# Optimization experiments

Measured on AMD Instinct MI355X. Metric: run time of the kernel, lower is better.

Reference implementation:

```python
import jax, jax.numpy as jnp
import numpy as np

B, C, H, W = 8, 384, 32, 32
KEYS, HEADS, U = 16, 4, 1
VS = C // HEADS
N = H * W
BN_EPS = 1e-5


def setup_inputs() -> dict:
    key = jax.random.key(0)
    ks = jax.random.split(key, 8)
    x = jax.random.normal(ks[0], (B, C, H, W), dtype=jnp.float32)
    # 1x1 convs (spectral-normalized in torch; SN only rescales the weight,
    # so a plain weight matrix computes the same functional form)
    Wq = jax.random.normal(ks[1], (KEYS * HEADS, C), dtype=jnp.float32) * 0.02
    Wk = jax.random.normal(ks[2], (KEYS * U, C), dtype=jnp.float32) * 0.02
    Wv = jax.random.normal(ks[3], (VS * U, C), dtype=jnp.float32) * 0.02
    # BatchNorm affine params (torch code xavier-inits weight, zeros bias)
    gamma_q = jax.random.normal(ks[4], (KEYS * HEADS,), dtype=jnp.float32)
    beta_q = jnp.zeros((KEYS * HEADS,), dtype=jnp.float32)
    gamma_v = jax.random.normal(ks[5], (VS * U,), dtype=jnp.float32)
    beta_v = jnp.zeros((VS * U,), dtype=jnp.float32)
    pos_emb = jax.random.normal(ks[6], (N, N, KEYS, U), dtype=jnp.float32)
    return {"x": x, "Wq": Wq, "Wk": Wk, "Wv": Wv,
            "gamma_q": gamma_q, "beta_q": beta_q,
            "gamma_v": gamma_v, "beta_v": beta_v,
            "pos_emb": pos_emb}


def _bn(z, gamma, beta):
    # z: (B, Ch, N); BatchNorm2d in training mode: biased batch stats over (B, N)
    mean = jnp.mean(z, axis=(0, 2), keepdims=True)
    var = jnp.var(z, axis=(0, 2), keepdims=True)
    zn = (z - mean) * jax.lax.rsqrt(var + BN_EPS)
    return zn * gamma[None, :, None] + beta[None, :, None]


def reference(x, Wq, Wk, Wv, gamma_q, beta_q, gamma_v, beta_v, pos_emb):
    xf = x.reshape(B, C, N)                       # 1x1 conv == per-pixel matmul
    q = jnp.einsum('oc,bcn->bon', Wq, xf)         # (B, KEYS*HEADS, N)
    k = jnp.einsum('oc,bcn->bon', Wk, xf)         # (B, KEYS*U, N)
    v = jnp.einsum('oc,bcn->bon', Wv, xf)         # (B, VS*U, N)
    q = _bn(q, gamma_q, beta_q)
    v = _bn(v, gamma_v, beta_v)
    q = q.reshape(B, HEADS, KEYS, N)
    k = k.reshape(B, U, KEYS, N)
    v = v.reshape(B, U, VS, N)
    k = jax.nn.softmax(k, axis=-1)
    lambdac = jnp.einsum('bukm,buvm->bkv', k, v)          # content lambda
    Yc = jnp.einsum('bhkn,bkv->bhvn', q, lambdac)
    lambdap = jnp.einsum('nmku,buvm->bnkv', pos_emb, v)   # position lambda (B,N,K,V)
    Yp = jnp.einsum('bhkn,bnkv->bhvn', q, lambdap)
    Y = (Yc + Yp).reshape(B, C, H, W)
    return Y
```

## Files before the change

kernel.cpp:

```cpp
#include <hip/hip_runtime.h>

typedef __attribute__((ext_vector_type(8))) short short8;
typedef __attribute__((ext_vector_type(16))) float floatx16;
typedef __attribute__((ext_vector_type(4))) float floatx4;
typedef unsigned short ushort16_t;
typedef unsigned int uint32;

#define BB 8
#define CC 384
#define NPIX 1024
#define TOTCH 176
#define BN_EPS 1e-5f

__device__ __forceinline__ ushort16_t f2bf(float x) {
    uint32 u = __float_as_uint(x);
    u += 0x7FFFu + ((u >> 16) & 1u);
    return (ushort16_t)(u >> 16);
}
__device__ __forceinline__ uint32 pk2(float a, float b) {
    uint32 ua = __float_as_uint(a); ua += 0x7FFFu + ((ua >> 16) & 1u);
    uint32 ub = __float_as_uint(b); ub += 0x7FFFu + ((ub >> 16) & 1u);
    return (ua >> 16) | (ub & 0xFFFF0000u);
}
__device__ __forceinline__ int div48(int x) {
    return (int)(((unsigned)x * 21846u) >> 20);
}
#define LGKM0_ONLY 0xC07F


__global__ __launch_bounds__(256) void k_xt(const float* __restrict__ x,
    const float* __restrict__ Wq, const float* __restrict__ Wk,
    const float* __restrict__ Wv,
    ushort16_t* __restrict__ xbf, ushort16_t* __restrict__ wbf)
{
    int bx = blockIdx.x, t = threadIdx.x;
    if (bx < 256) {
        __shared__ __align__(16) ushort16_t T[32 * 392];
        int col0 = bx * 32;
        int b = col0 >> 10, nbase = col0 & 1023;
        const float* xb = x + (size_t)b * (CC * NPIX) + nbase;
        #pragma unroll
        for (int j = 0; j < 12; ++j) {
            int idx = t + 256 * j;
            int c = idx >> 3, ng = idx & 7;
            float4 f = *(const float4*)(xb + (size_t)c * NPIX + ng * 4);
            int n = ng * 4;
            T[(n + 0) * 392 + c] = f2bf(f.x);
            T[(n + 1) * 392 + c] = f2bf(f.y);
            T[(n + 2) * 392 + c] = f2bf(f.z);
            T[(n + 3) * 392 + c] = f2bf(f.w);
        }
        __syncthreads();
        #pragma unroll
        for (int j = 0; j < 6; ++j) {
            int task = t + 256 * j;
            int col = div48(task);
            int ch  = task - col * 48;
            uint4 w = *(const uint4*)&T[col * 392 + ch * 8];
            *(uint4*)&xbf[(size_t)(col0 + col) * CC + ch * 8] = w;
        }
    } else {
        #pragma unroll
        for (int jj = 0; jj < 9; ++jj) {
            int idx8 = ((bx - 256) * 9 + jj) * 256 + t;
            int row = div48(idx8);
            int g   = idx8 - row * 48;
            float4 f0, f1;
            if (row < 176) {
                const float* src;
                if (row < 64)       src = Wq + (size_t)row * CC;
                else if (row < 80)  src = Wk + (size_t)(row - 64) * CC;
                else                src = Wv + (size_t)(row - 80) * CC;
                f0 = *(const float4*)(src + g * 8);
                f1 = *(const float4*)(src + g * 8 + 4);
            } else {
                f0.x = f0.y = f0.z = f0.w = 0.f;
                f1 = f0;
            }
            uint4 w;
            w.x = pk2(f0.x, f0.y); w.y = pk2(f0.z, f0.w);
            w.z = pk2(f1.x, f1.y); w.w = pk2(f1.z, f1.w);
            *(uint4*)&wbf[(size_t)row * CC + g * 8] = w;
        }
    }
}

__global__ __launch_bounds__(256) void k_proj(const ushort16_t* __restrict__ xbf,
    const ushort16_t* __restrict__ wbf, float* __restrict__ qkv)
{
    int t = threadIdx.x;
    int wave = t >> 6, lane = t & 63;
    int ct = blockIdx.x * 4 + wave;
    int r0 = blockIdx.y * 16;
    int col = ct * 16 + (lane & 15);
    int kh  = lane >> 4;
    const ushort16_t* ap = wbf + (size_t)(r0 + (lane & 15)) * CC + kh * 8;
    const ushort16_t* bp = xbf + (size_t)col * CC + kh * 8;
    floatx4 acc = {0.f, 0.f, 0.f, 0.f};
    short8 a0 = *(const short8*)ap;
    short8 b0 = *(const short8*)bp;
    #pragma unroll
    for (int k = 1; k < 12; ++k) {
        short8 a1 = *(const short8*)(ap + k * 32);
        short8 b1 = *(const short8*)(bp + k * 32);
        acc = __builtin_amdgcn_mfma_f32_16x16x32_bf16(a0, b0, acc, 0, 0, 0);
        a0 = a1; b0 = b1;
    }
    acc = __builtin_amdgcn_mfma_f32_16x16x32_bf16(a0, b0, acc, 0, 0, 0);
    int b = col >> 10, n = col & 1023;
    #pragma unroll
    for (int r = 0; r < 4; ++r) {
        int ch = r0 + (lane >> 4) * 4 + r;
        qkv[((size_t)b * TOTCH + ch) * NPIX + n] = acc[r];
    }
}

__global__ __launch_bounds__(256) void k_bnsm(const float* __restrict__ qkv,
    const float* __restrict__ gq, const float* __restrict__ bq,
    const float* __restrict__ gv, const float* __restrict__ bv,
    float* __restrict__ sA, float* __restrict__ sB, float* __restrict__ ksm)
{
    int bx = blockIdx.x, tid = threadIdx.x;
    int wid = tid >> 6, lane = tid & 63;
    if (bx < 160) {
        int ch = bx;
        int row; float gamma, beta;
        if (ch < 64) { row = ch; gamma = gq[ch]; beta = bq[ch]; }
        else { int j = ch - 64; row = 80 + j; gamma = gv[j]; beta = bv[j]; }
        float s = 0.f, ss = 0.f;
        #pragma unroll
        for (int j = 0; j < 8; ++j) {
            int i4 = tid + 256 * j;
            int b = i4 >> 8, n4 = i4 & 255;
            float4 f = *(const float4*)(qkv + ((size_t)b * TOTCH + row) * NPIX
                                            + n4 * 4);
            s  += f.x + f.y + f.z + f.w;
            ss += f.x * f.x + f.y * f.y + f.z * f.z + f.w * f.w;
        }
        #pragma unroll
        for (int off = 32; off > 0; off >>= 1) {
            s  += __shfl_down(s, off);
            ss += __shfl_down(ss, off);
        }
        __shared__ float rs[4], rss[4];
        if (lane == 0) { rs[wid] = s; rss[wid] = ss; }
        __syncthreads();
        if (tid == 0) {
            float S  = rs[0] + rs[1] + rs[2] + rs[3];
            float SS = rss[0] + rss[1] + rss[2] + rss[3];
            float inv = 1.f / (BB * NPIX);
            float mean = S * inv;
            float var  = SS * inv - mean * mean;
            float a = gamma * rsqrtf(var + BN_EPS);
            sA[row] = a;
            sB[row] = beta - mean * a;
        }
    } else {
        int idx = bx - 160;
        int kc = idx & 15, b = idx >> 4;
        const float* rowp = qkv + ((size_t)b * TOTCH + 64 + kc) * NPIX;
        float4 v4 = *(const float4*)(rowp + tid * 4);
        float v[4] = {v4.x, v4.y, v4.z, v4.w};
        float mx = fmaxf(fmaxf(v[0], v[1]), fmaxf(v[2], v[3]));
        #pragma unroll
        for (int off = 32; off > 0; off >>= 1) mx = fmaxf(mx, __shfl_down(mx, off));
        __shared__ float sm[4], ssum[4];
        if (lane == 0) sm[wid] = mx;
        __syncthreads();
        mx = fmaxf(fmaxf(sm[0], sm[1]), fmaxf(sm[2], sm[3]));
        float e[4], s = 0.f;
        #pragma unroll
        for (int j = 0; j < 4; ++j) { e[j] = __expf(v[j] - mx); s += e[j]; }
        #pragma unroll
        for (int off = 32; off > 0; off >>= 1) s += __shfl_down(s, off);
        if (lane == 0) ssum[wid] = s;
        __syncthreads();
        float inv = 1.f / (ssum[0] + ssum[1] + ssum[2] + ssum[3]);
        float4 o;
        o.x = e[0] * inv; o.y = e[1] * inv; o.z = e[2] * inv; o.w = e[3] * inv;
        *(float4*)(ksm + ((size_t)b * 16 + kc) * NPIX + tid * 4) = o;
    }
}

__global__ __launch_bounds__(256) void k_packlc(const float* __restrict__ qkv,
    const float* __restrict__ sA, const float* __restrict__ sB,
    const float* __restrict__ ksm,
    ushort16_t* __restrict__ qt_g, ushort16_t* __restrict__ vt_g,
    ushort16_t* __restrict__ lc_g)
{
    int bx = blockIdx.x, t = threadIdx.x;
    if (bx < 128) {
        int bh = t & 31, nn = (t >> 5) & 7;
        int n = bx * 8 + nn;
        int b = bh >> 2, h = bh & 3;
        float vals[16];
        #pragma unroll
        for (int k = 0; k < 16; ++k) {
            int ch = h * 16 + k;
            vals[k] = qkv[((size_t)b * TOTCH + ch) * NPIX + n] * sA[ch] + sB[ch];
        }
        uint4 w0, w1;
        w0.x = pk2(vals[0], vals[1]);  w0.y = pk2(vals[2], vals[3]);
        w0.z = pk2(vals[4], vals[5]);  w0.w = pk2(vals[6], vals[7]);
        w1.x = pk2(vals[8], vals[9]);  w1.y = pk2(vals[10], vals[11]);
        w1.z = pk2(vals[12], vals[13]); w1.w = pk2(vals[14], vals[15]);
        *(uint4*)&qt_g[(size_t)n * 512 + bh * 8]       = w0;
        *(uint4*)&qt_g[(size_t)n * 512 + 256 + bh * 8] = w1;
    } else if (bx < 512) {
        int gi = (bx - 128) * 256 + t;
        int m8 = gi & 127;
        int vg = (gi >> 7) % 96;
        int b  = gi / (96 * 128);
        int m  = m8 * 8;
        int row = 80 + vg;
        float a = sA[row], bb = sB[row];
        const float* p = qkv + ((size_t)b * TOTCH + row) * NPIX + m;
        float4 f0 = *(const float4*)p;
        float4 f1 = *(const float4*)(p + 4);
        uint4 w;
        w.x = pk2(f0.x * a + bb, f0.y * a + bb);
        w.y = pk2(f0.z * a + bb, f0.w * a + bb);
        w.z = pk2(f1.x * a + bb, f1.y * a + bb);
        w.w = pk2(f1.z * a + bb, f1.w * a + bb);
        int mt = m >> 5, mq = (m >> 3) & 3;
        int vhh = vg / 48, vtt = (vg % 48) >> 4, vl = vg & 15;
        size_t idx = ((((size_t)b * 32 + mt) * 2 + vhh) * 3 + vtt) * 512
                   + mq * 128 + vl * 8;
        *(uint4*)&vt_g[idx] = w;
    } else {
        int gi = bx - 512;
        int v = gi % 96, b = gi / 96;
        int row = 80 + v;
        float a = sA[row], bb = sB[row];
        const float* vp = qkv + ((size_t)b * TOTCH + row) * NPIX;
        const float* kp = ksm + (size_t)b * 16 * NPIX;
        float4 vv = *(const float4*)(vp + t * 4);
        float4 vhat;
        vhat.x = vv.x * a + bb; vhat.y = vv.y * a + bb;
        vhat.z = vv.z * a + bb; vhat.w = vv.w * a + bb;
        float acc[16];
        #pragma unroll
        for (int k = 0; k < 16; ++k) {
            float4 kk = *(const float4*)(kp + (size_t)k * NPIX + t * 4);
            acc[k] = kk.x * vhat.x + kk.y * vhat.y
                   + kk.z * vhat.z + kk.w * vhat.w;
        }
        #pragma unroll
        for (int k = 0; k < 16; ++k) {
            #pragma unroll
            for (int off = 32; off > 0; off >>= 1)
                acc[k] += __shfl_down(acc[k], off);
        }
        __shared__ float red[16][4];
        int wid = t >> 6, lane = t & 63;
        if (lane == 0) {
            #pragma unroll
            for (int k = 0; k < 16; ++k) red[k][wid] = acc[k];
        }
        __syncthreads();
        int vhh = v / 48, vtt = (v % 48) >> 4, vl = v & 15;
        size_t plane = ((size_t)(b * 2 + vhh) * 3 + vtt) * 512;
        if (t < 16) {
            int k = t;
            float val = red[k][0] + red[k][1] + red[k][2] + red[k][3];
            lc_g[plane + (k >> 3) * 128 + vl * 8 + (k & 7)] = f2bf(val);
        } else if (t < 18) {
            int mq = 2 + (t - 16);
            uint4 z; z.x = z.y = z.z = z.w = 0u;
            *(uint4*)&lc_g[plane + mq * 128 + vl * 8] = z;
        }
    }
}

__global__ __launch_bounds__(512, 2) void k_main(const float* __restrict__ pos,
    const ushort16_t* __restrict__ qt_g, const ushort16_t* __restrict__ vt_g,
    const ushort16_t* __restrict__ lc_g, float* __restrict__ out)
{
    __shared__ __align__(16) ushort16_t S_s[2][8192];
    int tid  = threadIdx.x;
    int lane = tid & 63;
    int wave = tid >> 6;
    int n0 = blockIdx.x * 8;
    int vh = blockIdx.y;

    int col1 = lane & 31, half = lane >> 5;
    int pb = col1 >> 2, ph = col1 & 3;
    int pplane = pb * 2 + (ph >> 1);
    int pf = pplane & 7;
    int pcb = ph & 1;
    int b2 = wave;

    short8 qfr = *(const short8*)(qt_g + (size_t)(n0 + wave) * 512
                                  + half * 256 + col1 * 8);

    floatx4 acc[2][3];
    #pragma unroll
    for (int hg = 0; hg < 2; ++hg)
        #pragma unroll
        for (int vt = 0; vt < 3; ++vt)
            acc[hg][vt] = floatx4{0.f, 0.f, 0.f, 0.f};

    floatx16 z16;
    #pragma unroll
    for (int i = 0; i < 16; ++i) z16[i] = 0.f;

    const float* pA = pos + ((size_t)(n0 + wave) * 1024 + col1) * 16 + half * 8;
    const ushort16_t* pV = vt_g + (size_t)b2 * 98304 + (size_t)vh * 1536
                         + lane * 8;

    float4 a0c = *(const float4*)(pA);
    float4 a1c = *(const float4*)(pA + 4);
    float4 a0n = *(const float4*)(pA + 512);
    float4 a1n = *(const float4*)(pA + 516);
    short8 av0 = *(const short8*)(pV);
    short8 av1 = *(const short8*)(pV + 512);
    short8 av2 = *(const short8*)(pV + 1024);

    for (int i = 0; i < 32; ++i) {
        float4 a0nn, a1nn;
        if (i < 30) {
            const float* p = pA + (size_t)(i + 2) * 512;
            a0nn = *(const float4*)p;
            a1nn = *(const float4*)(p + 4);
        }
        short8 nv0, nv1, nv2;
        if (i < 31) {
            const ushort16_t* vp = pV + (size_t)(i + 1) * 3072;
            nv0 = *(const short8*)(vp);
            nv1 = *(const short8*)(vp + 512);
            nv2 = *(const short8*)(vp + 1024);
        }
        {
            uint4 aw;
            aw.x = pk2(a0c.x, a0c.y); aw.y = pk2(a0c.z, a0c.w);
            aw.z = pk2(a1c.x, a1c.y); aw.w = pk2(a1c.z, a1c.w);
            short8 afr = *(short8*)&aw;
            floatx16 d = __builtin_amdgcn_mfma_f32_32x32x16_bf16(
                afr, qfr, z16, 0, 0, 0);
            int nx = wave ^ pf;
            ushort16_t* Sb = S_s[i & 1];
            #pragma unroll
            for (int q = 0; q < 4; ++q) {
                int c = q * 16 + pcb * 8 + nx;
                uint2 wv;
                wv.x = pk2(d[q * 4 + 0], d[q * 4 + 1]);
                wv.y = pk2(d[q * 4 + 2], d[q * 4 + 3]);
                *(uint2*)&Sb[pplane * 512 + c * 8 + half * 4] = wv;
            }
        }
        __builtin_amdgcn_s_waitcnt(LGKM0_ONLY);
        __builtin_amdgcn_s_barrier();
        {
            const ushort16_t* Sb = S_s[i & 1];
            #pragma unroll
            for (int hg = 0; hg < 2; ++hg) {
                int p2 = b2 * 2 + hg, f2 = p2 & 7;
                short8 bs = *(const short8*)&Sb[p2 * 512
                    + ((lane >> 4) * 16 + ((lane & 15) ^ f2)) * 8];
                acc[hg][0] = __builtin_amdgcn_mfma_f32_16x16x32_bf16(
                    av0, bs, acc[hg][0], 0, 0, 0);
                acc[hg][1] = __builtin_amdgcn_mfma_f32_16x16x32_bf16(
                    av1, bs, acc[hg][1], 0, 0, 0);
                acc[hg][2] = __builtin_amdgcn_mfma_f32_16x16x32_bf16(
                    av2, bs, acc[hg][2], 0, 0, 0);
            }
        }
        a0c = a0n; a1c = a1n;
        if (i < 30) { a0n = a0nn; a1n = a1nn; }
        if (i < 31) { av0 = nv0; av1 = nv1; av2 = nv2; }
    }

    {
        const ushort16_t* lsrc = lc_g + (size_t)(b2 * 2 + vh) * 1536 + lane * 8;
        short8 lv0 = *(const short8*)(lsrc);
        short8 lv1 = *(const short8*)(lsrc + 512);
        short8 lv2 = *(const short8*)(lsrc + 1024);
        __syncthreads();
        {
            int c = half * 16 + pcb * 8 + (wave ^ pf);
            *(short8*)&S_s[0][pplane * 512 + c * 8] = qfr;
            int zp = tid >> 5, zr = tid & 31;
            int zc = (2 + (zr >> 4)) * 16 + ((zr & 15) ^ (zp & 7));
            uint4 z; z.x = z.y = z.z = z.w = 0u;
            *(uint4*)&S_s[0][zp * 512 + zc * 8] = z;
        }
        __syncthreads();
        #pragma unroll
        for (int hg = 0; hg < 2; ++hg) {
            int p2 = b2 * 2 + hg, f2 = p2 & 7;
            short8 bs = *(const short8*)&S_s[0][p2 * 512
                + ((lane >> 4) * 16 + ((lane & 15) ^ f2)) * 8];
            acc[hg][0] = __builtin_amdgcn_mfma_f32_16x16x32_bf16(
                lv0, bs, acc[hg][0], 0, 0, 0);
            acc[hg][1] = __builtin_amdgcn_mfma_f32_16x16x32_bf16(
                lv1, bs, acc[hg][1], 0, 0, 0);
            acc[hg][2] = __builtin_amdgcn_mfma_f32_16x16x32_bf16(
                lv2, bs, acc[hg][2], 0, 0, 0);
        }
    }

    {
        int cn = lane & 15;
        int nloc = cn & 7;
        #pragma unroll
        for (int hg = 0; hg < 2; ++hg) {
            int h = hg * 2 + (cn >> 3);
            #pragma unroll
            for (int vt = 0; vt < 3; ++vt) {
                #pragma unroll
                for (int r = 0; r < 4; ++r) {
                    int v = vh * 48 + vt * 16 + (lane >> 4) * 4 + r;
                    out[(size_t)(b2 * 384 + h * 96 + v) * 1024 + n0 + nloc]
                        = acc[hg][vt][r];
                }
            }
        }
    }
}

extern "C" void kernel_launch(void* const* d_in, const int* in_sizes, int n_in,
                              void* d_out, int out_size, void* d_ws, size_t ws_size,
                              hipStream_t stream) {
    const float* x   = (const float*)d_in[0];
    const float* Wq  = (const float*)d_in[1];
    const float* Wk  = (const float*)d_in[2];
    const float* Wv  = (const float*)d_in[3];
    const float* gq  = (const float*)d_in[4];
    const float* bq  = (const float*)d_in[5];
    const float* gv  = (const float*)d_in[6];
    const float* bv  = (const float*)d_in[7];
    const float* pos = (const float*)d_in[8];
    float* out = (float*)d_out;
    float* ws  = (float*)d_ws;

    float* qkv = ws;
    float* sA  = ws + 1441792;
    float* sB  = ws + 1441968;
    float* ksm = ws + 1442144;
    ushort16_t* qt_g = (ushort16_t*)(ws + 1573216);
    ushort16_t* vt_g = (ushort16_t*)(ws + 1835360);
    ushort16_t* lc_g = (ushort16_t*)(ws + 2228576);
    ushort16_t* xbf  = (ushort16_t*)(ws + 2240864);
    ushort16_t* wbf  = (ushort16_t*)(ws + 3813728);

    k_xt<<<dim3(260), dim3(256), 0, stream>>>(x, Wq, Wk, Wv, xbf, wbf);
    k_proj<<<dim3(128, 11), dim3(256), 0, stream>>>(xbf, wbf, qkv);
    k_bnsm<<<dim3(288), dim3(256), 0, stream>>>(qkv, gq, bq, gv, bv, sA, sB, ksm);
    k_packlc<<<dim3(1280), dim3(256), 0, stream>>>(qkv, sA, sB, ksm,
                                                   qt_g, vt_g, lc_g);
    k_main<<<dim3(128, 2), dim3(512), 0, stream>>>(pos, qt_g, vt_g, lc_g, out);
}
```

Measured before the change: 179.3 us.

## Fuse x transpose/bf16 conversion into projection kernel via shared memory

The x transpose-and-convert step moves into the projection GEMM. Each block loads a 32-pixel slab of x into LDS as bf16 and computes all 11 output-row tiles from it, with waves splitting the row tiles. The xbf global round trip goes away, and the weight conversion becomes a tiny separate kernel. The grid shrinks from 1408 to 256 blocks, each doing more serial MFMA work, and the B operand is now read from LDS.

```diff
diff --git a/kernel.cpp b/kernel.cpp
--- a/kernel.cpp
+++ b/kernel.cpp
@@ -28,90 +28,81 @@
 #define LGKM0_ONLY 0xC07F
 
 
-__global__ __launch_bounds__(256) void k_xt(const float* __restrict__ x,
-    const float* __restrict__ Wq, const float* __restrict__ Wk,
-    const float* __restrict__ Wv,
-    ushort16_t* __restrict__ xbf, ushort16_t* __restrict__ wbf)
+__global__ __launch_bounds__(256) void k_wt(const float* __restrict__ Wq,
+    const float* __restrict__ Wk, const float* __restrict__ Wv,
+    ushort16_t* __restrict__ wbf)
 {
     int bx = blockIdx.x, t = threadIdx.x;
-    if (bx < 256) {
-        __shared__ __align__(16) ushort16_t T[32 * 392];
-        int col0 = bx * 32;
-        int b = col0 >> 10, nbase = col0 & 1023;
-        const float* xb = x + (size_t)b * (CC * NPIX) + nbase;
-        #pragma unroll
-        for (int j = 0; j < 12; ++j) {
-            int idx = t + 256 * j;
-            int c = idx >> 3, ng = idx & 7;
-            float4 f = *(const float4*)(xb + (size_t)c * NPIX + ng * 4);
-            int n = ng * 4;
-            T[(n + 0) * 392 + c] = f2bf(f.x);
-            T[(n + 1) * 392 + c] = f2bf(f.y);
-            T[(n + 2) * 392 + c] = f2bf(f.z);
-            T[(n + 3) * 392 + c] = f2bf(f.w);
-        }
-        __syncthreads();
-        #pragma unroll
-        for (int j = 0; j < 6; ++j) {
-            int task = t + 256 * j;
-            int col = div48(task);
-            int ch  = task - col * 48;
-            uint4 w = *(const uint4*)&T[col * 392 + ch * 8];
-            *(uint4*)&xbf[(size_t)(col0 + col) * CC + ch * 8] = w;
-        }
-    } else {
-        #pragma unroll
-        for (int jj = 0; jj < 9; ++jj) {
-            int idx8 = ((bx - 256) * 9 + jj) * 256 + t;
-            int row = div48(idx8);
-            int g   = idx8 - row * 48;
-            float4 f0, f1;
-            if (row < 176) {
-                const float* src;
-                if (row < 64)       src = Wq + (size_t)row * CC;
-                else if (row < 80)  src = Wk + (size_t)(row - 64) * CC;
-                else                src = Wv + (size_t)(row - 80) * CC;
-                f0 = *(const float4*)(src + g * 8);
-                f1 = *(const float4*)(src + g * 8 + 4);
-            } else {
-                f0.x = f0.y = f0.z = f0.w = 0.f;
-                f1 = f0;
-            }
-            uint4 w;
-            w.x = pk2(f0.x, f0.y); w.y = pk2(f0.z, f0.w);
-            w.z = pk2(f1.x, f1.y); w.w = pk2(f1.z, f1.w);
-            *(uint4*)&wbf[(size_t)row * CC + g * 8] = w;
-        }
-    }
-}
-
-__global__ __launch_bounds__(256) void k_proj(const ushort16_t* __restrict__ xbf,
+    #pragma unroll
+    for (int jj = 0; jj < 9; ++jj) {
+        int idx8 = (bx * 9 + jj) * 256 + t;
+        int row = div48(idx8);
+        int g   = idx8 - row * 48;
+        float4 f0, f1;
+        if (row < 176) {
+            const float* src;
+            if (row < 64)       src = Wq + (size_t)row * CC;
+            else if (row < 80)  src = Wk + (size_t)(row - 64) * CC;
+            else                src = Wv + (size_t)(row - 80) * CC;
+            f0 = *(const float4*)(src + g * 8);
+            f1 = *(const float4*)(src + g * 8 + 4);
+        } else {
+            f0.x = f0.y = f0.z = f0.w = 0.f;
+            f1 = f0;
+        }
+        uint4 w;
+        w.x = pk2(f0.x, f0.y); w.y = pk2(f0.z, f0.w);
+        w.z = pk2(f1.x, f1.y); w.w = pk2(f1.z, f1.w);
+        *(uint4*)&wbf[(size_t)row * CC + g * 8] = w;
+    }
+}
+
+__global__ __launch_bounds__(256) void k_proj(const float* __restrict__ x,
     const ushort16_t* __restrict__ wbf, float* __restrict__ qkv)
 {
-    int t = threadIdx.x;
+    __shared__ __align__(16) ushort16_t XT[32 * 392];
+    int bx = blockIdx.x, t = threadIdx.x;
+    int b = bx >> 5, nbase = (bx & 31) * 32;
+    const float* xb = x + (size_t)b * (CC * NPIX) + nbase;
+    #pragma unroll
+    for (int j = 0; j < 12; ++j) {
+        int idx = t + 256 * j;
+        int c = idx >> 3, ng = idx & 7;
+        float4 f = *(const float4*)(xb + (size_t)c * NPIX + ng * 4);
+        int col = ng * 4;
+        XT[(col + 0) * 392 + c] = f2bf(f.x);
+        XT[(col + 1) * 392 + c] = f2bf(f.y);
+        XT[(col + 2) * 392 + c] = f2bf(f.z);
+        XT[(col + 3) * 392 + c] = f2bf(f.w);
+    }
+    __syncthreads();
+
     int wave = t >> 6, lane = t & 63;
-    int ct = blockIdx.x * 4 + wave;
-    int r0 = blockIdx.y * 16;
-    int col = ct * 16 + (lane & 15);
-    int kh  = lane >> 4;
-    const ushort16_t* ap = wbf + (size_t)(r0 + (lane & 15)) * CC + kh * 8;
-    const ushort16_t* bp = xbf + (size_t)col * CC + kh * 8;
-    floatx4 acc = {0.f, 0.f, 0.f, 0.f};
-    short8 a0 = *(const short8*)ap;
-    short8 b0 = *(const short8*)bp;
-    #pragma unroll
-    for (int k = 1; k < 12; ++k) {
-        short8 a1 = *(const short8*)(ap + k * 32);
-        short8 b1 = *(const short8*)(bp + k * 32);
+    int ct = wave & 1;
+    int rs = wave >> 1;
+    int col1 = lane & 15, kq = lane >> 4;
+    const ushort16_t* bbase = &XT[(ct * 16 + col1) * 392 + kq * 8];
+    int n = nbase + ct * 16 + col1;
+
+    for (int r = rs; r < 11; r += 2) {
+        int r0 = r * 16;
+        const ushort16_t* ap = wbf + (size_t)(r0 + col1) * CC + kq * 8;
+        floatx4 acc = {0.f, 0.f, 0.f, 0.f};
+        short8 a0 = *(const short8*)ap;
+        short8 b0 = *(const short8*)bbase;
+        #pragma unroll
+        for (int k = 1; k < 12; ++k) {
+            short8 a1 = *(const short8*)(ap + k * 32);
+            short8 b1 = *(const short8*)(bbase + k * 32);
+            acc = __builtin_amdgcn_mfma_f32_16x16x32_bf16(a0, b0, acc, 0, 0, 0);
+            a0 = a1; b0 = b1;
+        }
         acc = __builtin_amdgcn_mfma_f32_16x16x32_bf16(a0, b0, acc, 0, 0, 0);
-        a0 = a1; b0 = b1;
-    }
-    acc = __builtin_amdgcn_mfma_f32_16x16x32_bf16(a0, b0, acc, 0, 0, 0);
-    int b = col >> 10, n = col & 1023;
-    #pragma unroll
-    for (int r = 0; r < 4; ++r) {
-        int ch = r0 + (lane >> 4) * 4 + r;
-        qkv[((size_t)b * TOTCH + ch) * NPIX + n] = acc[r];
+        #pragma unroll
+        for (int rr = 0; rr < 4; ++rr) {
+            int ch = r0 + kq * 4 + rr;
+            qkv[((size_t)b * TOTCH + ch) * NPIX + n] = acc[rr];
+        }
     }
 }
 
@@ -440,11 +431,10 @@
     ushort16_t* qt_g = (ushort16_t*)(ws + 1573216);
     ushort16_t* vt_g = (ushort16_t*)(ws + 1835360);
     ushort16_t* lc_g = (ushort16_t*)(ws + 2228576);
-    ushort16_t* xbf  = (ushort16_t*)(ws + 2240864);
     ushort16_t* wbf  = (ushort16_t*)(ws + 3813728);
 
-    k_xt<<<dim3(260), dim3(256), 0, stream>>>(x, Wq, Wk, Wv, xbf, wbf);
-    k_proj<<<dim3(128, 11), dim3(256), 0, stream>>>(xbf, wbf, qkv);
+    k_wt<<<dim3(4), dim3(256), 0, stream>>>(Wq, Wk, Wv, wbf);
+    k_proj<<<dim3(256), dim3(256), 0, stream>>>(x, wbf, qkv);
     k_bnsm<<<dim3(288), dim3(256), 0, stream>>>(qkv, gq, bq, gv, bv, sA, sB, ksm);
     k_packlc<<<dim3(1280), dim3(256), 0, stream>>>(qkv, sA, sB, ksm,
                                                    qt_g, vt_g, lc_g);
```

After: 169.5 us. -5.5%, faster.
